# Performance work log

Measured on AMD Instinct MI355X. Metric: run time of the kernel, lower is better.

## Reference

```python
import jax, jax.numpy as jnp
import numpy as np

NUM_HEADS = 12

def quick_gelu(z):
    return z * jax.nn.sigmoid(1.702 * z)

def setup_inputs() -> dict:
    key = jax.random.key(0)
    ks = jax.random.split(key, 8)
    B, Fn, P, E, R = 16, 12, 197, 768, 8
    s = 0.02
    return {
        "x": jax.random.normal(ks[0], (B * Fn, P, E), jnp.float32),
        "in_proj_weight": jax.random.normal(ks[1], (3 * E, E), jnp.float32) * s,
        "in_proj_bias": jnp.zeros((3 * E,), jnp.float32),
        "out_proj_weight": jax.random.normal(ks[2], (E, E), jnp.float32) * s,
        "out_proj_bias": jnp.zeros((E,), jnp.float32),
        "lora_a": jax.random.normal(ks[3], (R, E), jnp.float32) * s,
        "lora_b": jax.random.normal(ks[4], (3 * E, R), jnp.float32) * s,
        "down_w": jax.random.normal(ks[5], (R, E), jnp.float32) * s,
        "down_b": jnp.zeros((R,), jnp.float32),
        "up_w": jax.random.normal(ks[6], (E, R), jnp.float32) * s,
        "up_b": jnp.zeros((E,), jnp.float32),
        "b": B, "n_f": Fn, "token_len": P, "d_v": E,
    }

def reference(x, in_proj_weight, in_proj_bias, out_proj_weight, out_proj_bias,
              lora_a, lora_b, down_w, down_b, up_w, up_b,
              b, n_f, token_len, d_v):
    bsz, tgt, E = x.shape
    h = NUM_HEADS
    hd = E // h
    scaling = float(hd) ** -0.5

    # fused qkv + LoRA delta: [bsz, tgt, 3E]
    qkv = x @ in_proj_weight.T + in_proj_bias
    qkv = qkv + (x @ lora_a.T) @ lora_b.T
    qkv = qkv.reshape(bsz, tgt, 3, h, hd).transpose(2, 0, 3, 1, 4)
    q, k, v = qkv[0], qkv[1], qkv[2]  # each [bsz, h, tgt, hd]

    # CLS-token query per frame: (b f) h p d -> b h f d  (p=0)
    q_1 = q.reshape(b, n_f, h, tgt, hd).transpose(0, 2, 1, 3, 4)[:, :, :, 0, :]

    # per-frame local attention
    attn = jax.nn.softmax((scaling * q) @ k.transpose(0, 1, 3, 2), axis=-1)
    out = (attn @ v).transpose(0, 2, 1, 3).reshape(bsz, tgt, E)
    out = out @ out_proj_weight.T + out_proj_bias

    # cross-frame kv: (b f) h p d -> b h (f p) d
    k_all = k.reshape(b, n_f, h, tgt, hd).transpose(0, 2, 1, 3, 4).reshape(b, h, n_f * tgt, hd)
    v_all = v.reshape(b, n_f, h, tgt, hd).transpose(0, 2, 1, 3, 4).reshape(b, h, n_f * tgt, hd)

    attn_1 = jax.nn.softmax((scaling * q_1) @ k_all.transpose(0, 1, 3, 2), axis=-1)
    x_1 = (attn_1 @ v_all).transpose(0, 2, 1, 3).reshape(b, n_f, E)
    x_1 = x_1 @ out_proj_weight.T + out_proj_bias

    out = out.reshape(b, n_f, token_len, d_v)
    x_0 = out[:, :, 0, :]
    x_0 = quick_gelu(x_0 @ down_w.T + down_b) @ up_w.T + up_b
    out = out.at[:, :, 0, :].set(x_0 + x_1)
    return out.reshape(b * n_f, token_len, d_v)
```

## Files before the change

### kernel.cpp

```cpp
#include <hip/hip_runtime.h>
#include <hip/hip_bf16.h>

typedef __hip_bfloat16 bf16;
typedef __attribute__((ext_vector_type(8))) short bf16x8;
typedef __attribute__((ext_vector_type(4))) float f32x4;

#define NT   37824
#define MPAD 37888
#define EDIM 768
#define N3   2304
#define TP   197
#define NB   16
#define NF   12
#define NH   12
#define HD   64
#define SCALE 0.125f
#define KALL 2364

__device__ __forceinline__ float bits2f(unsigned short u) {
    unsigned int v = ((unsigned int)u) << 16;
    return __uint_as_float(v);
}
__device__ __forceinline__ float b2f(bf16 v) { return __bfloat162float(v); }

__device__ __forceinline__ unsigned short bhi(float x) {
    union { bf16 b; unsigned short u; } cv; cv.b = __float2bfloat16(x); return cv.u;
}
__device__ __forceinline__ unsigned short blo(float x, unsigned short h) {
    float hf = __uint_as_float(((unsigned int)h) << 16);
    union { bf16 b; unsigned short u; } cv; cv.b = __float2bfloat16(x - hf); return cv.u;
}

__device__ __forceinline__ void storeC(float* p, float v) { *p = v; }
__device__ __forceinline__ void storeC(bf16* p, float v) { *p = __float2bfloat16(v); }

__device__ __forceinline__ void gload_lds16(const bf16* g, bf16* l) {
    __builtin_amdgcn_global_load_lds(
        (const __attribute__((address_space(1))) void*)g,
        (__attribute__((address_space(3))) void*)l,
        16, 0, 0);
}

__global__ __launch_bounds__(256) void lora_mid_kernel(const float* __restrict__ x,
        const float* __restrict__ la, float* __restrict__ mid) {
    int t = blockIdx.x * 4 + (threadIdx.x >> 6);
    int lane = threadIdx.x & 63;
    if (t >= NT) return;
    float acc[8];
#pragma unroll
    for (int r = 0; r < 8; r++) acc[r] = 0.f;
    const float* xr = x + (size_t)t * EDIM;
    for (int e = lane; e < EDIM; e += 64) {
        float xv = xr[e];
#pragma unroll
        for (int r = 0; r < 8; r++) acc[r] += xv * la[r * EDIM + e];
    }
#pragma unroll
    for (int r = 0; r < 8; r++) {
        float v = acc[r];
#pragma unroll
        for (int off = 32; off >= 1; off >>= 1) v += __shfl_xor(v, off, 64);
        if (lane == 0) mid[(size_t)t * 8 + r] = v;
    }
}

__global__ __launch_bounds__(256) void split_w_kernel(const float* __restrict__ w,
        bf16* __restrict__ o, int rows) {
    int idx = blockIdx.x * 256 + threadIdx.x;
    int total = rows * 192;
    if (idx >= total) return;
    int r = idx / 192, c = (idx - r * 192) * 4;
    float4 v = *reinterpret_cast<const float4*>(w + (size_t)r * 768 + c);
    ushort4 hi, lo;
    hi.x = bhi(v.x); hi.y = bhi(v.y); hi.z = bhi(v.z); hi.w = bhi(v.w);
    lo.x = blo(v.x, hi.x); lo.y = blo(v.y, hi.y); lo.z = blo(v.z, hi.z); lo.w = blo(v.w, hi.w);
    *(ushort4*)(o + (size_t)r * 1536 + c) = hi;
    *(ushort4*)(o + (size_t)r * 1536 + 768 + c) = lo;
}

template <typename OT, bool LORA>
__global__ __launch_bounds__(256) void mfma_gemm_kernel(const bf16* __restrict__ A, int lda,
        const bf16* __restrict__ W, const float* __restrict__ bias,
        const float* __restrict__ mid, const float* __restrict__ lb,
        OT* __restrict__ C, int M, int N, int KV) {
    __shared__ bf16 As[2][128 * 64];
    __shared__ bf16 Bs[2][128 * 64];
    const int tid = threadIdx.x;
    const int w = tid >> 6, lane = tid & 63;
    const int lr = lane & 15, lg = lane >> 4;
    const int wr = w >> 1, wc = w & 1;

    const int gx = gridDim.x;
    const int nwg = gx * gridDim.y;
    const int flat = blockIdx.y * gx + blockIdx.x;
    const int cpx = nwg >> 3;
    const int lid = (flat & 7) * cpx + (flat >> 3);
    const int m0 = (lid / gx) * 128, n0 = (lid % gx) * 128;

    f32x4 acc[4][4];
#pragma unroll
    for (int i = 0; i < 4; i++)
#pragma unroll
        for (int j = 0; j < 4; j++) acc[i][j] = (f32x4){0.f, 0.f, 0.f, 0.f};

    const int brs = lane >> 3;
    const int bcsw = ((lane & 7) ^ brs) << 3;

    const int nt = KV / 64;

    {
        const int aOff = 0, wOff = 0;
#pragma unroll
        for (int j = 0; j < 4; j++) {
            int seg = j * 4 + w;
            int row = seg * 8 + brs;
            gload_lds16(A + (size_t)(m0 + row) * lda + aOff + bcsw, &As[0][seg * 512]);
            gload_lds16(W + (size_t)(n0 + row) * 1536 + wOff + bcsw, &Bs[0][seg * 512]);
        }
    }
    __syncthreads();

    int cur = 0;
    for (int t = 0; t < nt; ++t) {
        if (t + 1 < nt) {
            const int k0 = (t + 1) * 64;
            const int aOff = (k0 >= 768) ? k0 - 768 : k0;
            const int wOff = (k0 >= 1536) ? k0 - 1536 : k0;
            const int nxt = cur ^ 1;
#pragma unroll
            for (int j = 0; j < 4; j++) {
                int seg = j * 4 + w;
                int row = seg * 8 + brs;
                gload_lds16(A + (size_t)(m0 + row) * lda + aOff + bcsw, &As[nxt][seg * 512]);
                gload_lds16(W + (size_t)(n0 + row) * 1536 + wOff + bcsw, &Bs[nxt][seg * 512]);
            }
        }
        bf16x8 a[4][2], b[4][2];
#pragma unroll
        for (int mf = 0; mf < 4; mf++) {
            int row = wr * 64 + mf * 16 + lr;
            int sw = (row & 7) << 4;
            a[mf][0] = *(const bf16x8*)((const char*)&As[cur][0] + row * 128 + ((lg * 16) ^ sw));
            a[mf][1] = *(const bf16x8*)((const char*)&As[cur][0] + row * 128 + ((64 + lg * 16) ^ sw));
        }
#pragma unroll
        for (int nf = 0; nf < 4; nf++) {
            int row = wc * 64 + nf * 16 + lr;
            int sw = (row & 7) << 4;
            b[nf][0] = *(const bf16x8*)((const char*)&Bs[cur][0] + row * 128 + ((lg * 16) ^ sw));
            b[nf][1] = *(const bf16x8*)((const char*)&Bs[cur][0] + row * 128 + ((64 + lg * 16) ^ sw));
        }
        __builtin_amdgcn_s_setprio(1);
#pragma unroll
        for (int mf = 0; mf < 4; mf++)
#pragma unroll
            for (int nf = 0; nf < 4; nf++) {
                acc[mf][nf] = __builtin_amdgcn_mfma_f32_16x16x32_bf16(a[mf][0], b[nf][0], acc[mf][nf], 0, 0, 0);
                acc[mf][nf] = __builtin_amdgcn_mfma_f32_16x16x32_bf16(a[mf][1], b[nf][1], acc[mf][nf], 0, 0, 0);
            }
        __builtin_amdgcn_s_setprio(0);
        __syncthreads();
        cur ^= 1;
    }
#pragma unroll
    for (int mf = 0; mf < 4; mf++) {
#pragma unroll
        for (int r = 0; r < 4; r++) {
            int m = m0 + wr * 64 + mf * 16 + lg * 4 + r;
            if (m < M) {
                float mr[8];
                if constexpr (LORA) {
                    float4 u0 = *reinterpret_cast<const float4*>(mid + (size_t)m * 8);
                    float4 u1 = *reinterpret_cast<const float4*>(mid + (size_t)m * 8 + 4);
                    mr[0] = u0.x; mr[1] = u0.y; mr[2] = u0.z; mr[3] = u0.w;
                    mr[4] = u1.x; mr[5] = u1.y; mr[6] = u1.z; mr[7] = u1.w;
                }
#pragma unroll
                for (int nf = 0; nf < 4; nf++) {
                    int n = n0 + wc * 64 + nf * 16 + lr;
                    float v = acc[mf][nf][r] + bias[n];
                    if constexpr (LORA) {
                        const float4 l0 = *reinterpret_cast<const float4*>(lb + (size_t)n * 8);
                        const float4 l1 = *reinterpret_cast<const float4*>(lb + (size_t)n * 8 + 4);
                        v += mr[0] * l0.x + mr[1] * l0.y + mr[2] * l0.z + mr[3] * l0.w
                           + mr[4] * l1.x + mr[5] * l1.y + mr[6] * l1.z + mr[7] * l1.w;
                    }
                    storeC(C + (size_t)m * N + n, v);
                }
            }
        }
    }
}

__global__ __launch_bounds__(256) void attn_kernel(const bf16* __restrict__ qkv,
        bf16* __restrict__ ao) {
    __shared__ bf16 Ks[208 * 64];
    __shared__ bf16 Vt[64 * 208];
    __shared__ bf16 Ps[4][16 * 208];
    const int bb = blockIdx.x / NH;
    const int h = blockIdx.x % NH;
    const bf16* base = qkv + (size_t)bb * TP * N3;
    const int tid = threadIdx.x;
    const int w = tid >> 6, lane = tid & 63;
    const int lr = lane & 15, lg = lane >> 4;

    for (int idx = tid; idx < 208 * 16; idx += 256) {
        int row = idx >> 4, d4 = (idx & 15) * 4;
        ushort4 v = make_ushort4(0, 0, 0, 0);
        if (row < TP)
            v = *(const ushort4*)(base + (size_t)row * N3 + EDIM + h * 64 + d4);
        *(ushort4*)((char*)Ks + ((row * 128 + d4 * 2) ^ ((row & 7) << 4))) = v;
    }
    for (int g = w; g < 52; g += 4) {
        int kk0 = g * 4;
        int d = lane;
        const bf16* vb = base + (size_t)kk0 * N3 + 2 * EDIM + h * 64 + d;
        unsigned short t0 = 0, t1 = 0, t2 = 0, t3 = 0;
        if (kk0 + 0 < TP) t0 = *(const unsigned short*)(vb);
        if (kk0 + 1 < TP) t1 = *(const unsigned short*)(vb + N3);
        if (kk0 + 2 < TP) t2 = *(const unsigned short*)(vb + 2 * N3);
        if (kk0 + 3 < TP) t3 = *(const unsigned short*)(vb + 3 * N3);
        ushort4 v; v.x = t0; v.y = t1; v.z = t2; v.w = t3;
        *(ushort4*)((char*)Vt + ((d * 416 + kk0 * 2) ^ ((d & 7) << 4))) = v;
    }
    __syncthreads();

    bf16* Pw = &Ps[w][0];

    for (int qt = w; qt < 13; qt += 4) {
        int q = qt * 16 + lr; if (q > TP - 1) q = TP - 1;
        const bf16* qp = base + (size_t)q * N3 + h * 64 + lg * 8;
        bf16x8 qa0 = *(const bf16x8*)qp;
        bf16x8 qa1 = *(const bf16x8*)(qp + 32);

        f32x4 sf[13];
#pragma unroll
        for (int f = 0; f < 13; f++) {
            int row = f * 16 + lr;
            int swz = (row & 7) << 4;
            bf16x8 kb0 = *(const bf16x8*)((const char*)Ks + ((row * 128 + lg * 16) ^ swz));
            bf16x8 kb1 = *(const bf16x8*)((const char*)Ks + ((row * 128 + 64 + lg * 16) ^ swz));
            f32x4 c = {0.f, 0.f, 0.f, 0.f};
            c = __builtin_amdgcn_mfma_f32_16x16x32_bf16(qa0, kb0, c, 0, 0, 0);
            c = __builtin_amdgcn_mfma_f32_16x16x32_bf16(qa1, kb1, c, 0, 0, 0);
            sf[f] = c;
        }

        float mx[4] = {-1e30f, -1e30f, -1e30f, -1e30f};
#pragma unroll
        for (int f = 0; f < 13; f++) {
#pragma unroll
            for (int r = 0; r < 4; r++) {
                float s = sf[f][r] * SCALE;
                if (f == 12 && lr >= 5) s = -1e30f;
                sf[f][r] = s;
                mx[r] = fmaxf(mx[r], s);
            }
        }
#pragma unroll
        for (int off = 8; off >= 1; off >>= 1) {
#pragma unroll
            for (int r = 0; r < 4; r++) mx[r] = fmaxf(mx[r], __shfl_xor(mx[r], off, 64));
        }
        float lsum[4] = {0.f, 0.f, 0.f, 0.f};
#pragma unroll
        for (int f = 0; f < 13; f++) {
#pragma unroll
            for (int r = 0; r < 4; r++) {
                float e = __expf(sf[f][r] - mx[r]);
                sf[f][r] = e;
                lsum[r] += e;
            }
        }
#pragma unroll
        for (int off = 8; off >= 1; off >>= 1) {
#pragma unroll
            for (int r = 0; r < 4; r++) lsum[r] += __shfl_xor(lsum[r], off, 64);
        }
        float inv[4];
#pragma unroll
        for (int r = 0; r < 4; r++) inv[r] = 1.f / lsum[r];

#pragma unroll
        for (int f = 0; f < 13; f++) {
#pragma unroll
            for (int r = 0; r < 4; r++) {
                int row = lg * 4 + r;
                int col = f * 16 + lr;
                *(bf16*)((char*)Pw + ((row * 416 + col * 2) ^ ((row & 7) << 4))) =
                    __float2bfloat16(sf[f][r]);
            }
        }

        f32x4 of[4];
#pragma unroll
        for (int dt = 0; dt < 4; dt++) of[dt] = (f32x4){0.f, 0.f, 0.f, 0.f};
#pragma unroll
        for (int ks = 0; ks < 7; ks++) {
            int k0 = ks * 32 + lg * 8;
            bool ok = (k0 < 208);
            bf16x8 pa = {0, 0, 0, 0, 0, 0, 0, 0};
            if (ok)
                pa = *(const bf16x8*)((const char*)Pw + ((lr * 416 + k0 * 2) ^ ((lr & 7) << 4)));
#pragma unroll
            for (int dt = 0; dt < 4; dt++) {
                bf16x8 vb = {0, 0, 0, 0, 0, 0, 0, 0};
                if (ok) {
                    int d = dt * 16 + lr;
                    vb = *(const bf16x8*)((const char*)Vt + ((d * 416 + k0 * 2) ^ ((d & 7) << 4)));
                }
                of[dt] = __builtin_amdgcn_mfma_f32_16x16x32_bf16(pa, vb, of[dt], 0, 0, 0);
            }
        }

#pragma unroll
        for (int dt = 0; dt < 4; dt++) {
#pragma unroll
            for (int r = 0; r < 4; r++) {
                int qq = qt * 16 + lg * 4 + r;
                if (qq < TP)
                    ao[((size_t)bb * TP + qq) * EDIM + h * 64 + dt * 16 + lr] =
                        __float2bfloat16(of[dt][r] * inv[r]);
            }
        }
    }
}

__global__ __launch_bounds__(256) void xattn_kernel(const bf16* __restrict__ qkv,
        float* __restrict__ x1p) {
    __shared__ float q1[NF][64];
    __shared__ bf16 Ks[128][64];
    __shared__ bf16 Vs[128][64];
    __shared__ float sc[NF][128];
    __shared__ float Oacc[NF][64];
    __shared__ float mrow[NF], lrow[NF], arow[NF];
    const int b = blockIdx.x / NH, h = blockIdx.x % NH;
    const int tid = threadIdx.x;
    for (int idx = tid; idx < NF * 64; idx += 256) {
        int f = idx >> 6, d = idx & 63;
        q1[f][d] = b2f(qkv[(size_t)((b * NF + f) * TP) * N3 + h * 64 + d]);
        Oacc[f][d] = 0.f;
    }
    if (tid < NF) { mrow[tid] = -1e30f; lrow[tid] = 0.f; }
    __syncthreads();
    const int w = tid >> 6, lane = tid & 63;
    for (int kk0 = 0; kk0 < KALL; kk0 += 128) {
        for (int idx = tid; idx < 128 * 16; idx += 256) {
            int r = idx >> 4, d4 = (idx & 15) * 4;
            int kk = kk0 + r;
            if (kk < KALL) {
                int f = kk / TP, pp = kk - f * TP;
                const bf16* src = qkv + (size_t)((b * NF + f) * TP + pp) * N3 + h * 64 + d4;
                *(ushort4*)&Ks[r][d4] = *(const ushort4*)(src + 768);
                *(ushort4*)&Vs[r][d4] = *(const ushort4*)(src + 1536);
            } else {
                ushort4 z; z.x = z.y = z.z = z.w = 0;
                *(ushort4*)&Ks[r][d4] = z;
                *(ushort4*)&Vs[r][d4] = z;
            }
        }
        __syncthreads();
        for (int idx = tid; idx < NF * 128; idx += 256) {
            int f = idx >> 7, r = idx & 127;
            float s = -1e30f;
            if (kk0 + r < KALL) {
                const bf16* kr = &Ks[r][0];
                float a = 0.f;
#pragma unroll
                for (int d2 = 0; d2 < 32; d2++) {
                    unsigned int u = *reinterpret_cast<const unsigned int*>(kr + 2 * d2);
                    a += q1[f][2 * d2] * __uint_as_float(u << 16);
                    a += q1[f][2 * d2 + 1] * __uint_as_float(u & 0xffff0000u);
                }
                s = a * SCALE;
            }
            sc[f][r] = s;
        }
        __syncthreads();
        for (int qi = 0; qi < 3; qi++) {
            int f = qi * 4 + w;
            float s0 = sc[f][lane], s1v = sc[f][lane + 64];
            float mx = fmaxf(s0, s1v);
#pragma unroll
            for (int off = 32; off >= 1; off >>= 1) mx = fmaxf(mx, __shfl_xor(mx, off, 64));
            float mold = mrow[f];
            float mnew = fmaxf(mold, mx);
            float e0 = __expf(s0 - mnew), e1 = __expf(s1v - mnew);
            float ls = e0 + e1;
#pragma unroll
            for (int off = 32; off >= 1; off >>= 1) ls += __shfl_xor(ls, off, 64);
            sc[f][lane] = e0; sc[f][lane + 64] = e1;
            if (lane == 0) {
                float alpha = __expf(mold - mnew);
                arow[f] = alpha;
                lrow[f] = lrow[f] * alpha + ls;
                mrow[f] = mnew;
            }
        }
        __syncthreads();
        for (int idx = tid; idx < NF * 64; idx += 256) {
            int f = idx >> 6, d = idx & 63;
            float o = Oacc[f][d] * arow[f];
#pragma unroll 4
            for (int r = 0; r < 128; r++)
                o += sc[f][r] * b2f(Vs[r][d]);
            Oacc[f][d] = o;
        }
        __syncthreads();
    }
    for (int idx = tid; idx < NF * 64; idx += 256) {
        int f = idx >> 6, d = idx & 63;
        x1p[(size_t)(b * NF + f) * EDIM + h * 64 + d] = Oacc[f][d] / lrow[f];
    }
}

__global__ __launch_bounds__(256) void cls_kernel(float* __restrict__ out,
        const float* __restrict__ x1p, const float* __restrict__ Wout, const float* __restrict__ ob,
        const float* __restrict__ dw, const float* __restrict__ db,
        const float* __restrict__ uw, const float* __restrict__ ub) {
    __shared__ float x0s[EDIM], x1s[EDIM], gs[8];
    const int bfi = blockIdx.x;
    float* row = out + (size_t)bfi * TP * EDIM;
    const int tid = threadIdx.x;
    for (int i = tid; i < EDIM; i += 256) {
        x0s[i] = row[i];
        x1s[i] = x1p[(size_t)bfi * EDIM + i];
    }
    __syncthreads();
    {
        int r = tid >> 5, sl = tid & 31;
        float pr = 0.f;
        for (int e = sl; e < EDIM; e += 32) pr += x0s[e] * dw[r * EDIM + e];
#pragma unroll
        for (int off = 16; off >= 1; off >>= 1) pr += __shfl_xor(pr, off, 64);
        if (sl == 0) gs[r] = pr + db[r];
    }
    __syncthreads();
    float act[8];
#pragma unroll
    for (int r = 0; r < 8; r++) { float g = gs[r]; act[r] = g / (1.f + __expf(-1.702f * g)); }
    for (int j = tid; j < EDIM; j += 256) {
        float y = ub[j] + ob[j];
        const float4 u0 = *reinterpret_cast<const float4*>(uw + (size_t)j * 8);
        const float4 u1 = *reinterpret_cast<const float4*>(uw + (size_t)j * 8 + 4);
        y += act[0] * u0.x + act[1] * u0.y + act[2] * u0.z + act[3] * u0.w
           + act[4] * u1.x + act[5] * u1.y + act[6] * u1.z + act[7] * u1.w;
        const float* wr = Wout + (size_t)j * EDIM;
        float s = 0.f;
        for (int e = 0; e < EDIM; e += 4) {
            float4 wv = *reinterpret_cast<const float4*>(wr + e);
            s += x1s[e] * wv.x + x1s[e + 1] * wv.y + x1s[e + 2] * wv.z + x1s[e + 3] * wv.w;
        }
        y += s;
        row[j] = y;
    }
}

extern "C" void kernel_launch(void* const* d_in, const int* in_sizes, int n_in,
                              void* d_out, int out_size, void* d_ws, size_t ws_size,
                              hipStream_t stream) {
    (void)in_sizes; (void)n_in; (void)out_size; (void)ws_size;
    const float* x   = (const float*)d_in[0];
    const float* ipw = (const float*)d_in[1];
    const float* ipb = (const float*)d_in[2];
    const float* opw = (const float*)d_in[3];
    const float* opb = (const float*)d_in[4];
    const float* la  = (const float*)d_in[5];
    const float* lb  = (const float*)d_in[6];
    const float* dw  = (const float*)d_in[7];
    const float* db  = (const float*)d_in[8];
    const float* uw  = (const float*)d_in[9];
    const float* ub  = (const float*)d_in[10];
    float* out = (float*)d_out;

    char* wsb = (char*)d_ws;
    bf16* qkv = (bf16*)wsb;                       wsb += (size_t)NT * N3 * sizeof(bf16);
    bf16* ao  = (bf16*)wsb;                       wsb += (size_t)MPAD * EDIM * sizeof(bf16);
    bf16* xs  = (bf16*)wsb;                       wsb += (size_t)MPAD * 1536 * sizeof(bf16);
    bf16* W1  = (bf16*)wsb;                       wsb += (size_t)N3 * 1536 * sizeof(bf16);
    bf16* W2  = (bf16*)wsb;                       wsb += (size_t)EDIM * 1536 * sizeof(bf16);
    float* mid = (float*)wsb;                     wsb += (size_t)NT * 8 * sizeof(float);
    float* x1p = (float*)wsb;                     wsb += (size_t)NB * NF * EDIM * sizeof(float);

    split_w_kernel<<<(N3 * 192 + 255) / 256, 256, 0, stream>>>(ipw, W1, N3);
    split_w_kernel<<<(EDIM * 192 + 255) / 256, 256, 0, stream>>>(opw, W2, EDIM);
    split_w_kernel<<<(NT * 192 + 255) / 256, 256, 0, stream>>>(x, xs, NT);
    lora_mid_kernel<<<NT / 4, 256, 0, stream>>>(x, la, mid);
    mfma_gemm_kernel<bf16, true><<<dim3(N3 / 128, MPAD / 128), 256, 0, stream>>>(
        xs, 1536, W1, ipb, mid, lb, qkv, NT, N3, 2304);
    attn_kernel<<<192 * NH, 256, 0, stream>>>(qkv, ao);
    xattn_kernel<<<NB * NH, 256, 0, stream>>>(qkv, x1p);
    mfma_gemm_kernel<float, false><<<dim3(EDIM / 128, MPAD / 128), 256, 0, stream>>>(
        ao, 768, W2, opb, nullptr, nullptr, out, NT, EDIM, 1536);
    cls_kernel<<<NB * NF, 256, 0, stream>>>(out, x1p, opw, opb, dw, db, uw, ub);
}
```

Measured before the change: 1.541 ms.

## Enlarge GEMM tiles to 256x256 with 8 waves and two-stage prefetch

Raises the MFMA GEMM workgroup tile from 128x128 with 4 waves to 256x256 with 8 waves. Each wave now computes a 128x64 sub-tile in two halves, with explicit barriers between them. Loads are prefetched two K-steps ahead using vmcnt waits instead of one step, and the XCD block remapping is changed to handle grid sizes not divisible by 8. The larger tiles cut global and LDS reload traffic per FLOP, at the cost of doubled LDS (128KB), more accumulator registers and fewer workgroups, which may leave CUs idle on the 768-wide output GEMM.

```diff
diff --git a/kernel.cpp b/kernel.cpp
--- a/kernel.cpp
+++ b/kernel.cpp
@@ -79,76 +79,72 @@
 }
 
 template <typename OT, bool LORA>
-__global__ __launch_bounds__(256) void mfma_gemm_kernel(const bf16* __restrict__ A, int lda,
+__global__ __launch_bounds__(512, 2) void mfma_gemm_kernel(const bf16* __restrict__ A, int lda,
         const bf16* __restrict__ W, const float* __restrict__ bias,
         const float* __restrict__ mid, const float* __restrict__ lb,
         OT* __restrict__ C, int M, int N, int KV) {
-    __shared__ bf16 As[2][128 * 64];
-    __shared__ bf16 Bs[2][128 * 64];
+    __shared__ bf16 As[2][256 * 64];
+    __shared__ bf16 Bs[2][256 * 64];
     const int tid = threadIdx.x;
     const int w = tid >> 6, lane = tid & 63;
     const int lr = lane & 15, lg = lane >> 4;
-    const int wr = w >> 1, wc = w & 1;
+    const int wr = w >> 2, wc = w & 3;
 
     const int gx = gridDim.x;
     const int nwg = gx * gridDim.y;
     const int flat = blockIdx.y * gx + blockIdx.x;
-    const int cpx = nwg >> 3;
-    const int lid = (flat & 7) * cpx + (flat >> 3);
-    const int m0 = (lid / gx) * 128, n0 = (lid % gx) * 128;
-
-    f32x4 acc[4][4];
-#pragma unroll
-    for (int i = 0; i < 4; i++)
+    const int xcd = flat & 7, loc = flat >> 3;
+    const int q = nwg >> 3, rmd = nwg & 7;
+    const int lid = (xcd < rmd ? xcd * (q + 1) : rmd * (q + 1) + (xcd - rmd) * q) + loc;
+    const int m0 = (lid / gx) * 256, n0 = (lid % gx) * 256;
+
+    f32x4 acc[8][4];
+#pragma unroll
+    for (int i = 0; i < 8; i++)
 #pragma unroll
         for (int j = 0; j < 4; j++) acc[i][j] = (f32x4){0.f, 0.f, 0.f, 0.f};
 
     const int brs = lane >> 3;
     const int bcsw = ((lane & 7) ^ brs) << 3;
 
+    auto STAGE = [&](bf16* dA, bf16* dB, int aO, int wO) {
+#pragma unroll
+        for (int j = 0; j < 4; ++j) {
+            int rA = w * 32 + j * 8;
+            gload_lds16(A + (size_t)(m0 + rA + brs) * lda + aO + bcsw, dA + rA * 64);
+            gload_lds16(W + (size_t)(n0 + rA + brs) * 1536 + wO + bcsw, dB + rA * 64);
+        }
+    };
+
     const int nt = KV / 64;
-
+    STAGE(&As[0][0], &Bs[0][0], 0, 0);
     {
-        const int aOff = 0, wOff = 0;
-#pragma unroll
-        for (int j = 0; j < 4; j++) {
-            int seg = j * 4 + w;
-            int row = seg * 8 + brs;
-            gload_lds16(A + (size_t)(m0 + row) * lda + aOff + bcsw, &As[0][seg * 512]);
-            gload_lds16(W + (size_t)(n0 + row) * 1536 + wOff + bcsw, &Bs[0][seg * 512]);
-        }
-    }
-    __syncthreads();
+        const int k1 = 64;
+        STAGE(&As[1][0], &Bs[1][0], (k1 >= 768) ? k1 - 768 : k1, k1);
+    }
+    asm volatile("s_waitcnt vmcnt(8)" ::: "memory");
+    __builtin_amdgcn_sched_barrier(0);
+    __builtin_amdgcn_s_barrier();
+    __builtin_amdgcn_sched_barrier(0);
 
     int cur = 0;
     for (int t = 0; t < nt; ++t) {
-        if (t + 1 < nt) {
-            const int k0 = (t + 1) * 64;
-            const int aOff = (k0 >= 768) ? k0 - 768 : k0;
-            const int wOff = (k0 >= 1536) ? k0 - 1536 : k0;
-            const int nxt = cur ^ 1;
-#pragma unroll
-            for (int j = 0; j < 4; j++) {
-                int seg = j * 4 + w;
-                int row = seg * 8 + brs;
-                gload_lds16(A + (size_t)(m0 + row) * lda + aOff + bcsw, &As[nxt][seg * 512]);
-                gload_lds16(W + (size_t)(n0 + row) * 1536 + wOff + bcsw, &Bs[nxt][seg * 512]);
-            }
-        }
+        const char* pA = (const char*)&As[cur][0];
+        const char* pB = (const char*)&Bs[cur][0];
         bf16x8 a[4][2], b[4][2];
-#pragma unroll
-        for (int mf = 0; mf < 4; mf++) {
-            int row = wr * 64 + mf * 16 + lr;
-            int sw = (row & 7) << 4;
-            a[mf][0] = *(const bf16x8*)((const char*)&As[cur][0] + row * 128 + ((lg * 16) ^ sw));
-            a[mf][1] = *(const bf16x8*)((const char*)&As[cur][0] + row * 128 + ((64 + lg * 16) ^ sw));
-        }
 #pragma unroll
         for (int nf = 0; nf < 4; nf++) {
             int row = wc * 64 + nf * 16 + lr;
             int sw = (row & 7) << 4;
-            b[nf][0] = *(const bf16x8*)((const char*)&Bs[cur][0] + row * 128 + ((lg * 16) ^ sw));
-            b[nf][1] = *(const bf16x8*)((const char*)&Bs[cur][0] + row * 128 + ((64 + lg * 16) ^ sw));
+            b[nf][0] = *(const bf16x8*)(pB + row * 128 + ((lg * 16) ^ sw));
+            b[nf][1] = *(const bf16x8*)(pB + row * 128 + ((64 + lg * 16) ^ sw));
+        }
+#pragma unroll
+        for (int mf = 0; mf < 4; mf++) {
+            int row = wr * 128 + mf * 16 + lr;
+            int sw = (row & 7) << 4;
+            a[mf][0] = *(const bf16x8*)(pA + row * 128 + ((lg * 16) ^ sw));
+            a[mf][1] = *(const bf16x8*)(pA + row * 128 + ((64 + lg * 16) ^ sw));
         }
         __builtin_amdgcn_s_setprio(1);
 #pragma unroll
@@ -159,14 +155,47 @@
                 acc[mf][nf] = __builtin_amdgcn_mfma_f32_16x16x32_bf16(a[mf][1], b[nf][1], acc[mf][nf], 0, 0, 0);
             }
         __builtin_amdgcn_s_setprio(0);
-        __syncthreads();
+        __builtin_amdgcn_sched_barrier(0);
+        __builtin_amdgcn_s_barrier();
+        __builtin_amdgcn_sched_barrier(0);
+#pragma unroll
+        for (int mf = 0; mf < 4; mf++) {
+            int row = wr * 128 + 64 + mf * 16 + lr;
+            int sw = (row & 7) << 4;
+            a[mf][0] = *(const bf16x8*)(pA + row * 128 + ((lg * 16) ^ sw));
+            a[mf][1] = *(const bf16x8*)(pA + row * 128 + ((64 + lg * 16) ^ sw));
+        }
+        __builtin_amdgcn_s_setprio(1);
+#pragma unroll
+        for (int mf = 0; mf < 4; mf++)
+#pragma unroll
+            for (int nf = 0; nf < 4; nf++) {
+                acc[4 + mf][nf] = __builtin_amdgcn_mfma_f32_16x16x32_bf16(a[mf][0], b[nf][0], acc[4 + mf][nf], 0, 0, 0);
+                acc[4 + mf][nf] = __builtin_amdgcn_mfma_f32_16x16x32_bf16(a[mf][1], b[nf][1], acc[4 + mf][nf], 0, 0, 0);
+            }
+        __builtin_amdgcn_s_setprio(0);
+        __builtin_amdgcn_sched_barrier(0);
+        __builtin_amdgcn_s_barrier();
+        __builtin_amdgcn_sched_barrier(0);
+        if (t + 2 < nt) {
+            const int k2 = (t + 2) * 64;
+            STAGE(&As[cur][0], &Bs[cur][0],
+                  (k2 >= 768) ? k2 - 768 : k2,
+                  (k2 >= 1536) ? k2 - 1536 : k2);
+            asm volatile("s_waitcnt vmcnt(8)" ::: "memory");
+        } else {
+            asm volatile("s_waitcnt vmcnt(0)" ::: "memory");
+        }
+        __builtin_amdgcn_sched_barrier(0);
+        __builtin_amdgcn_s_barrier();
+        __builtin_amdgcn_sched_barrier(0);
         cur ^= 1;
     }
 #pragma unroll
-    for (int mf = 0; mf < 4; mf++) {
+    for (int mf = 0; mf < 8; mf++) {
 #pragma unroll
         for (int r = 0; r < 4; r++) {
-            int m = m0 + wr * 64 + mf * 16 + lg * 4 + r;
+            int m = m0 + wr * 128 + mf * 16 + lg * 4 + r;
             if (m < M) {
                 float mr[8];
                 if constexpr (LORA) {
@@ -486,11 +515,11 @@
     split_w_kernel<<<(EDIM * 192 + 255) / 256, 256, 0, stream>>>(opw, W2, EDIM);
     split_w_kernel<<<(NT * 192 + 255) / 256, 256, 0, stream>>>(x, xs, NT);
     lora_mid_kernel<<<NT / 4, 256, 0, stream>>>(x, la, mid);
-    mfma_gemm_kernel<bf16, true><<<dim3(N3 / 128, MPAD / 128), 256, 0, stream>>>(
+    mfma_gemm_kernel<bf16, true><<<dim3(N3 / 256, MPAD / 256), 512, 0, stream>>>(
         xs, 1536, W1, ipb, mid, lb, qkv, NT, N3, 2304);
     attn_kernel<<<192 * NH, 256, 0, stream>>>(qkv, ao);
     xattn_kernel<<<NB * NH, 256, 0, stream>>>(qkv, x1p);
-    mfma_gemm_kernel<float, false><<<dim3(EDIM / 128, MPAD / 128), 256, 0, stream>>>(
+    mfma_gemm_kernel<float, false><<<dim3(EDIM / 256, MPAD / 256), 512, 0, stream>>>(
         ao, 768, W2, opb, nullptr, nullptr, out, NT, EDIM, 1536);
     cls_kernel<<<NB * NF, 256, 0, stream>>>(out, x1p, opw, opb, dw, db, uw, ub);
 }
```

After: 1.514 ms. About the same (-1.7%).
